# Kernel optimization log

Hardware: AMD Instinct MI355X
Metric: run time of the kernel (lower is better)

The kernel has to match this reference:

```python
import jax, jax.numpy as jnp
import numpy as np

NUM_EMBED = 1024
NUM_HEADS = 16
NUM_LAYER = 8
BLOCK_SIZE = 1024
VOCAB = 32000
B, T = 4, 1024
HEAD_SIZE = NUM_EMBED // NUM_HEADS


def _ln(x, g, b, eps=1e-5):
    mu = jnp.mean(x, axis=-1, keepdims=True)
    var = jnp.var(x, axis=-1, keepdims=True)
    return (x - mu) * jax.lax.rsqrt(var + eps) * g + b


def setup_inputs() -> dict:
    key = jax.random.key(0)
    ks = jax.random.split(key, 16)
    C, L, V = NUM_EMBED, NUM_LAYER, VOCAB
    std = 0.02
    n = lambda k, shp: jax.random.normal(k, shp, jnp.float32) * std
    return {
        "x": jax.random.randint(ks[0], (B, T), 0, V),
        "tok_emb": n(ks[1], (V, C)),
        "pos_emb": n(ks[2], (BLOCK_SIZE, C)),
        "Wq": n(ks[3], (L, C, C)),
        "Wk": n(ks[4], (L, C, C)),
        "Wv": n(ks[5], (L, C, C)),
        "Wproj": n(ks[6], (L, C, C)),
        "bproj": jnp.zeros((L, C), jnp.float32),
        "ln1_g": jnp.ones((L, C), jnp.float32),
        "ln1_b": jnp.zeros((L, C), jnp.float32),
        "ln2_g": jnp.ones((L, C), jnp.float32),
        "ln2_b": jnp.zeros((L, C), jnp.float32),
        "W1": n(ks[7], (L, C, 4 * C)),
        "b1": jnp.zeros((L, 4 * C), jnp.float32),
        "W2": n(ks[8], (L, 4 * C, C)),
        "b2": jnp.zeros((L, C), jnp.float32),
        "lnf_g": jnp.ones((C,), jnp.float32),
        "lnf_b": jnp.zeros((C,), jnp.float32),
        "Whead": n(ks[9], (C, V)),
    }


def _forward(x, tok_emb, pos_emb, Wq, Wk, Wv, Wproj, bproj,
             ln1_g, ln1_b, ln2_g, ln2_b, W1, b1, W2, b2,
             lnf_g, lnf_b, Whead):
    Bc, Tc = x.shape
    H, hs = NUM_HEADS, HEAD_SIZE
    h = tok_emb[x] + pos_emb[:Tc]  # [B,T,C]
    causal = jnp.tril(jnp.ones((Tc, Tc), bool))
    neg_inf = jnp.finfo(h.dtype).min
    for l in range(NUM_LAYER):
        xn = _ln(h, ln1_g[l], ln1_b[l])
        q = (xn @ Wq[l]).reshape(Bc, Tc, H, hs)
        k = (xn @ Wk[l]).reshape(Bc, Tc, H, hs)
        v = (xn @ Wv[l]).reshape(Bc, Tc, H, hs)
        att = jnp.einsum('bqhd,bkhd->bhqk', q, k) * (hs ** -0.5)
        att = jnp.where(causal, att, neg_inf)
        att = jax.nn.softmax(att, axis=-1)  # dropout p=0 in eval
        o = jnp.einsum('bhqk,bkhd->bqhd', att, v).reshape(Bc, Tc, H * hs)
        h = h + o @ Wproj[l] + bproj[l]
        xn = _ln(h, ln2_g[l], ln2_b[l])
        h = h + jax.nn.relu(xn @ W1[l] + b1[l]) @ W2[l] + b2[l]
    h = _ln(h, lnf_g, lnf_b)
    return h @ Whead  # logits [B,T,V]


def reference(x, tok_emb, pos_emb, Wq, Wk, Wv, Wproj, bproj,
              ln1_g, ln1_b, ln2_g, ln2_b, W1, b1, W2, b2,
              lnf_g, lnf_b, Whead):
    return _forward(x, tok_emb, pos_emb, Wq, Wk, Wv, Wproj, bproj,
                    ln1_g, ln1_b, ln2_g, ln2_b, W1, b1, W2, b2,
                    lnf_g, lnf_b, Whead)
```

## Files before the change

kernel.cpp:

```cpp
#include <hip/hip_runtime.h>
#include <stdint.h>
#include <stddef.h>

#define C_DIM 1024
#define T_DIM 1024
#define B_DIM 4
#define L_DIM 8
#define V_DIM 32000
#define HS 64
#define NHEAD 16
#define NROWS (B_DIM * T_DIM)
#define LDQ   3072

typedef __bf16 bf16_t;
typedef __attribute__((ext_vector_type(8))) __bf16 bf16x8;
typedef __attribute__((ext_vector_type(4))) __bf16 bf16x4;
typedef __attribute__((ext_vector_type(4))) float f32x4;
typedef unsigned int u32;
typedef unsigned short u16;

static __device__ __forceinline__ f32x4 mfma16(bf16x8 a, bf16x8 b, f32x4 c) {
    return __builtin_amdgcn_mfma_f32_16x16x32_bf16(a, b, c, 0, 0, 0);
}

static __device__ __forceinline__ void gl_lds16(const bf16_t* g, bf16_t* l) {
    __builtin_amdgcn_global_load_lds(
        (const __attribute__((address_space(1))) u32*)(const void*)g,
        (__attribute__((address_space(3))) u32*)(void*)l, 16, 0, 0);
}

__global__ __launch_bounds__(256) void embed_kernel(
    const int* __restrict__ x, const float* __restrict__ tok,
    const float* __restrict__ pos, float* __restrict__ h) {
    int idx = blockIdx.x * 256 + threadIdx.x;
    int row = idx >> 8;
    int c4  = (idx & 255) * 4;
    int t   = row & (T_DIM - 1);
    int tk  = x[row];
    float4 a = *(const float4*)(tok + (size_t)tk * C_DIM + c4);
    float4 p = *(const float4*)(pos + (size_t)t * C_DIM + c4);
    float4 r;
    r.x = a.x + p.x; r.y = a.y + p.y; r.z = a.z + p.z; r.w = a.w + p.w;
    *(float4*)(h + (size_t)row * C_DIM + c4) = r;
}

static __device__ __forceinline__ void wtr_tile(
    const float* __restrict__ in, bf16_t* __restrict__ out,
    int K, int N, int n0, int k0, int tid) {
    __shared__ float t[64][65];
    int tx = tid & 63, tw = tid >> 6;
#pragma unroll 4
    for (int i = 0; i < 16; ++i) {
        int k = tw * 16 + i;
        t[k][tx] = in[(size_t)(k0 + k) * N + n0 + tx];
    }
    __syncthreads();
#pragma unroll 4
    for (int i = 0; i < 16; ++i) {
        int n = tw * 16 + i;
        out[(size_t)(n0 + n) * K + k0 + tx] = (bf16_t)t[tx][n];
    }
}

__global__ __launch_bounds__(256) void wtr_kernel(
    const float* __restrict__ in, bf16_t* __restrict__ out, int K, int N) {
    wtr_tile(in, out, K, N, blockIdx.x * 64, blockIdx.y * 64, threadIdx.x);
}

__global__ __launch_bounds__(256) void wtr_layer_kernel(
    const float* __restrict__ Wq, const float* __restrict__ Wk,
    const float* __restrict__ Wv, const float* __restrict__ Wp,
    const float* __restrict__ W1, const float* __restrict__ W2,
    bf16_t* __restrict__ qkvT, bf16_t* __restrict__ projT,
    bf16_t* __restrict__ w1T, bf16_t* __restrict__ w2T) {
    int b = blockIdx.x;
    const float* in; bf16_t* out; int K, N, tn, tk;
    if (b < 1024) {
        int which = b >> 8, t = b & 255;
        in  = which == 0 ? Wq : which == 1 ? Wk : which == 2 ? Wv : Wp;
        out = which < 3 ? qkvT + (size_t)which * C_DIM * C_DIM : projT;
        K = C_DIM; N = C_DIM; tn = t & 15; tk = t >> 4;
    } else if (b < 2048) {
        int t = b - 1024; in = W1; out = w1T;
        K = C_DIM; N = 4 * C_DIM; tn = t & 63; tk = t >> 6;
    } else {
        int t = b - 2048; in = W2; out = w2T;
        K = 4 * C_DIM; N = C_DIM; tn = t & 15; tk = t >> 4;
    }
    wtr_tile(in, out, K, N, tn * 64, tk * 64, threadIdx.x);
}

__global__ __launch_bounds__(256) void ln_kernel(
    const float* __restrict__ x, const float* __restrict__ gam,
    const float* __restrict__ bet, bf16_t* __restrict__ out) {
    int wave = threadIdx.x >> 6, lane = threadIdx.x & 63;
    int row  = blockIdx.x * 4 + wave;
    const float* xr = x + (size_t)row * C_DIM;
    float4 v[4];
    float s = 0.f, sq = 0.f;
#pragma unroll
    for (int i = 0; i < 4; ++i) {
        v[i] = *(const float4*)(xr + i * 256 + lane * 4);
        s  += v[i].x + v[i].y + v[i].z + v[i].w;
        sq += v[i].x * v[i].x + v[i].y * v[i].y + v[i].z * v[i].z + v[i].w * v[i].w;
    }
#pragma unroll
    for (int m = 1; m < 64; m <<= 1) {
        s  += __shfl_xor(s, m);
        sq += __shfl_xor(sq, m);
    }
    float mu  = s * (1.f / 1024.f);
    float var = sq * (1.f / 1024.f) - mu * mu;
    float rs  = rsqrtf(var + 1e-5f);
    bf16_t* orow = out + (size_t)row * C_DIM;
#pragma unroll
    for (int i = 0; i < 4; ++i) {
        int c = i * 256 + lane * 4;
        float4 g4 = *(const float4*)(gam + c);
        float4 b4 = *(const float4*)(bet + c);
        bf16x4 o;
        o[0] = (bf16_t)((v[i].x - mu) * rs * g4.x + b4.x);
        o[1] = (bf16_t)((v[i].y - mu) * rs * g4.y + b4.y);
        o[2] = (bf16_t)((v[i].z - mu) * rs * g4.z + b4.z);
        o[3] = (bf16_t)((v[i].w - mu) * rs * g4.w + b4.w);
        *(bf16x4*)(orow + c) = o;
    }
}

template <int MODE>
__global__ __launch_bounds__(256) void gemm_kernel(
    const bf16_t* __restrict__ A, const bf16_t* __restrict__ Bt,
    const float* __restrict__ bias, void* __restrict__ Cout,
    int M, int N, int K) {
    __shared__ bf16_t Asm[2][128 * 32];
    __shared__ bf16_t Bsm[2][128 * 32];

    const int tid  = threadIdx.x;
    const int nwg  = gridDim.x;
    int bid = blockIdx.x;
    if ((nwg & 7) == 0) {
        int cpx = nwg >> 3;
        bid = (bid & 7) * cpx + (bid >> 3);
    }
    const int MT = M >> 7;
    const int mt = bid % MT, nt = bid / MT;
    const int mbase = mt << 7, nbase = nt << 7;
    const int wave = tid >> 6, lane = tid & 63;
    const int lr = lane & 15, lg = lane >> 4;
    const int wm = wave >> 1, wn = wave & 1;
    const int NK = K >> 5;

    const int srow = lane >> 2;
    const int ssw  = (((lane & 3) ^ ((lane >> 3) & 3)) << 3);
    const bf16_t* aRow = A  + (size_t)(mbase + wave * 32 + srow) * K + ssw;
    const bf16_t* bRow = Bt + (size_t)(nbase + wave * 32 + srow) * K + ssw;
    const int ldsW = wave * 1024;

#define STAGE(buf, kt)                                                        \
    do {                                                                      \
        const bf16_t* ag = aRow + (size_t)(kt) * 32;                          \
        const bf16_t* bg = bRow + (size_t)(kt) * 32;                          \
        gl_lds16(ag,            &Asm[buf][ldsW]);                             \
        gl_lds16(ag + 16 * K,   &Asm[buf][ldsW + 512]);                       \
        gl_lds16(bg,            &Bsm[buf][ldsW]);                             \
        gl_lds16(bg + 16 * K,   &Bsm[buf][ldsW + 512]);                       \
    } while (0)

    STAGE(0, 0);
    __syncthreads();

    f32x4 acc[4][4] = {};
    const int rsw = ((lg ^ ((lr >> 1) & 3)) << 3);
    int buf = 0;
    for (int kt = 0; kt < NK; ++kt) {
        if (kt + 1 < NK) STAGE(buf ^ 1, kt + 1);
        bf16x8 af[4], bfr[4];
#pragma unroll
        for (int i = 0; i < 4; ++i)
            af[i] = *(const bf16x8*)&Asm[buf][(wm * 64 + i * 16 + lr) * 32 + rsw];
#pragma unroll
        for (int j = 0; j < 4; ++j)
            bfr[j] = *(const bf16x8*)&Bsm[buf][(wn * 64 + j * 16 + lr) * 32 + rsw];
#pragma unroll
        for (int i = 0; i < 4; ++i)
#pragma unroll
            for (int j = 0; j < 4; ++j)
                acc[i][j] = mfma16(af[i], bfr[j], acc[i][j]);
        __syncthreads();
        buf ^= 1;
    }
#undef STAGE

    float bj[4];
#pragma unroll
    for (int j = 0; j < 4; ++j)
        bj[j] = bias ? bias[nbase + wn * 64 + j * 16 + lr] : 0.0f;
#pragma unroll
    for (int i = 0; i < 4; ++i) {
#pragma unroll
        for (int j = 0; j < 4; ++j) {
            int col = nbase + wn * 64 + j * 16 + lr;
#pragma unroll
            for (int e = 0; e < 4; ++e) {
                int row = mbase + wm * 64 + i * 16 + lg * 4 + e;
                float val = acc[i][j][e] + bj[j];
                size_t off = (size_t)row * N + col;
                if (MODE == 0) {
                    ((bf16_t*)Cout)[off] = (bf16_t)val;
                } else if (MODE == 1) {
                    ((bf16_t*)Cout)[off] = (bf16_t)fmaxf(val, 0.0f);
                } else if (MODE == 2) {
                    ((float*)Cout)[off] += val;
                } else {
                    __builtin_nontemporal_store(val, &((float*)Cout)[off]);
                }
            }
        }
    }
}

__global__ __launch_bounds__(256) void attn_kernel(
    const bf16_t* __restrict__ Qb, const bf16_t* __restrict__ Kb,
    const bf16_t* __restrict__ Vb, bf16_t* __restrict__ Ob) {
    __shared__ bf16_t Ksm[2][64][72];
    __shared__ bf16_t Vsm[2][64][72];
    __shared__ bf16_t Psm[4][32][72];

    const int tid  = threadIdx.x;
    const int bid  = blockIdx.x;
    const int qt   = 7 - (bid >> 6);
    const int bh   = bid & 63;
    const int hh   = bh & 15;
    const int bb   = bh >> 4;
    const int wave = tid >> 6, lane = tid & 63;
    const int lr = lane & 15, lg = lane >> 4;
    const int qbase = qt * 128 + wave * 32;
    const size_t basei = ((size_t)bb * T_DIM) * LDQ + hh * HS;
    const size_t baseo = ((size_t)bb * T_DIM) * C_DIM + hh * HS;

    bf16x8 qf[2][2];
#pragma unroll
    for (int rb = 0; rb < 2; ++rb) {
        const bf16_t* qrow = Qb + basei + (size_t)(qbase + rb * 16 + lr) * LDQ;
        qf[rb][0] = *(const bf16x8*)(qrow + lg * 8);
        qf[rb][1] = *(const bf16x8*)(qrow + 32 + lg * 8);
    }

    f32x4 o[2][4] = {};
    float m_run[2][4], psum[2][4];
#pragma unroll
    for (int rb = 0; rb < 2; ++rb)
#pragma unroll
        for (int e = 0; e < 4; ++e) { m_run[rb][e] = -1e30f; psum[rb][e] = 0.f; }

    const int krow = tid >> 2, kc = (tid & 3) * 8;
    const bf16_t* kgp = Kb + basei + (size_t)krow * LDQ + kc;
    const int vds = (tid & 7) * 8, vkg = (tid >> 3) * 2;
    const bf16_t* vgp0 = Vb + basei + (size_t)vkg * LDQ + vds;
    const bf16_t* vgp1 = vgp0 + LDQ;

    const int nkt = 2 * qt + 2;

    uint4 k0r, k1r, v0r, v1r;
    k0r = *(const uint4*)(kgp);
    k1r = *(const uint4*)(kgp + 32);
    v0r = *(const uint4*)(vgp0);
    v1r = *(const uint4*)(vgp1);
    *(uint4*)&Ksm[0][krow][kc]      = k0r;
    *(uint4*)&Ksm[0][krow][kc + 32] = k1r;
    {
        const u16* e0 = (const u16*)&v0r;
        const u16* e1 = (const u16*)&v1r;
#pragma unroll
        for (int j = 0; j < 8; ++j)
            *(u32*)&Vsm[0][vds + j][vkg] = (u32)e0[j] | ((u32)e1[j] << 16);
    }
    __syncthreads();

    const float SCL = 0.18033688011112042f;
    for (int kt = 0; kt < nkt; ++kt) {
        const int c = kt & 1;
        if (kt + 1 < nkt) {
            const size_t go = (size_t)(kt + 1) * 64 * LDQ;
            k0r = *(const uint4*)(kgp + go);
            k1r = *(const uint4*)(kgp + go + 32);
            v0r = *(const uint4*)(vgp0 + go);
            v1r = *(const uint4*)(vgp1 + go);
        }

        f32x4 s[2][4];
        __builtin_amdgcn_s_setprio(1);
#pragma unroll
        for (int kk = 0; kk < 4; ++kk) {
            bf16x8 kf0 = *(const bf16x8*)&Ksm[c][kk * 16 + lr][lg * 8];
            bf16x8 kf1 = *(const bf16x8*)&Ksm[c][kk * 16 + lr][32 + lg * 8];
#pragma unroll
            for (int rb = 0; rb < 2; ++rb) {
                f32x4 z = {};
                z = mfma16(qf[rb][0], kf0, z);
                z = mfma16(qf[rb][1], kf1, z);
                s[rb][kk] = z;
            }
        }
        __builtin_amdgcn_s_setprio(0);
        if (kt * 64 + 63 > qbase) {
#pragma unroll
            for (int rb = 0; rb < 2; ++rb)
#pragma unroll
                for (int kk = 0; kk < 4; ++kk)
#pragma unroll
                    for (int e = 0; e < 4; ++e) {
                        int key = kt * 64 + kk * 16 + lr;
                        int qi  = qbase + rb * 16 + lg * 4 + e;
                        float v = s[rb][kk][e] * SCL;
                        s[rb][kk][e] = (key <= qi) ? v : -1e30f;
                    }
        } else {
#pragma unroll
            for (int rb = 0; rb < 2; ++rb)
#pragma unroll
                for (int kk = 0; kk < 4; ++kk)
#pragma unroll
                    for (int e = 0; e < 4; ++e)
                        s[rb][kk][e] *= SCL;
        }

#pragma unroll
        for (int rb = 0; rb < 2; ++rb) {
#pragma unroll
            for (int e = 0; e < 4; ++e) {
                float v = fmaxf(fmaxf(s[rb][0][e], s[rb][1][e]),
                                fmaxf(s[rb][2][e], s[rb][3][e]));
                v = fmaxf(v, __shfl_xor(v, 1));
                v = fmaxf(v, __shfl_xor(v, 2));
                v = fmaxf(v, __shfl_xor(v, 4));
                v = fmaxf(v, __shfl_xor(v, 8));
                float mo = m_run[rb][e];
                if (v > mo + 8.f) {
                    float alpha = exp2f(mo - v);
                    m_run[rb][e] = v;
                    psum[rb][e] *= alpha;
#pragma unroll
                    for (int db = 0; db < 4; ++db)
                        o[rb][db][e] *= alpha;
                }
                float mn = m_run[rb][e];
                float p0 = exp2f(s[rb][0][e] - mn);
                float p1 = exp2f(s[rb][1][e] - mn);
                float p2 = exp2f(s[rb][2][e] - mn);
                float p3 = exp2f(s[rb][3][e] - mn);
                int qrow = rb * 16 + lg * 4 + e;
                Psm[wave][qrow][lr]      = (bf16_t)p0;
                Psm[wave][qrow][16 + lr] = (bf16_t)p1;
                Psm[wave][qrow][32 + lr] = (bf16_t)p2;
                Psm[wave][qrow][48 + lr] = (bf16_t)p3;
                psum[rb][e] += (p0 + p1) + (p2 + p3);
            }
        }

        asm volatile("s_waitcnt lgkmcnt(0)" ::: "memory");
        bf16x8 pf[2][2];
#pragma unroll
        for (int rb = 0; rb < 2; ++rb)
#pragma unroll
            for (int h2 = 0; h2 < 2; ++h2)
                pf[rb][h2] = *(const bf16x8*)&Psm[wave][rb * 16 + lr][h2 * 32 + lg * 8];
        __builtin_amdgcn_s_setprio(1);
#pragma unroll
        for (int h2 = 0; h2 < 2; ++h2)
#pragma unroll
            for (int db = 0; db < 4; ++db) {
                bf16x8 vf = *(const bf16x8*)&Vsm[c][db * 16 + lr][h2 * 32 + lg * 8];
#pragma unroll
                for (int rb = 0; rb < 2; ++rb)
                    o[rb][db] = mfma16(pf[rb][h2], vf, o[rb][db]);
            }
        __builtin_amdgcn_s_setprio(0);

        if (kt + 1 < nkt) {
            const int w = c ^ 1;
            *(uint4*)&Ksm[w][krow][kc]      = k0r;
            *(uint4*)&Ksm[w][krow][kc + 32] = k1r;
            const u16* e0 = (const u16*)&v0r;
            const u16* e1 = (const u16*)&v1r;
#pragma unroll
            for (int j = 0; j < 8; ++j)
                *(u32*)&Vsm[w][vds + j][vkg] = (u32)e0[j] | ((u32)e1[j] << 16);
        }
        __syncthreads();
    }

#pragma unroll
    for (int rb = 0; rb < 2; ++rb)
#pragma unroll
        for (int e = 0; e < 4; ++e) {
            float l = psum[rb][e];
            l += __shfl_xor(l, 1);
            l += __shfl_xor(l, 2);
            l += __shfl_xor(l, 4);
            l += __shfl_xor(l, 8);
            float inv = 1.0f / l;
            bf16_t* orow = Ob + baseo + (size_t)(qbase + rb * 16 + lg * 4 + e) * C_DIM;
#pragma unroll
            for (int db = 0; db < 4; ++db)
                orow[db * 16 + lr] = (bf16_t)(o[rb][db][e] * inv);
        }
}

extern "C" void kernel_launch(void* const* d_in, const int* in_sizes, int n_in,
                              void* d_out, int out_size, void* d_ws, size_t ws_size,
                              hipStream_t stream) {
    const int*   x      = (const int*)d_in[0];
    const float* tok    = (const float*)d_in[1];
    const float* pos    = (const float*)d_in[2];
    const float* Wq     = (const float*)d_in[3];
    const float* Wk     = (const float*)d_in[4];
    const float* Wv     = (const float*)d_in[5];
    const float* Wproj  = (const float*)d_in[6];
    const float* bproj  = (const float*)d_in[7];
    const float* ln1_g  = (const float*)d_in[8];
    const float* ln1_b  = (const float*)d_in[9];
    const float* ln2_g  = (const float*)d_in[10];
    const float* ln2_b  = (const float*)d_in[11];
    const float* W1     = (const float*)d_in[12];
    const float* b1     = (const float*)d_in[13];
    const float* W2     = (const float*)d_in[14];
    const float* b2     = (const float*)d_in[15];
    const float* lnf_g  = (const float*)d_in[16];
    const float* lnf_b  = (const float*)d_in[17];
    const float* Whead  = (const float*)d_in[18];
    float* out = (float*)d_out;

    char* ws = (char*)d_ws;
    float*  h    = (float*)ws;   ws += (size_t)NROWS * C_DIM * 4;
    bf16_t* xn   = (bf16_t*)ws;  ws += (size_t)NROWS * C_DIM * 2;
    bf16_t* qkvb = (bf16_t*)ws;  ws += (size_t)NROWS * LDQ * 2;
    bf16_t* ob   = (bf16_t*)ws;  ws += (size_t)NROWS * C_DIM * 2;
    bf16_t* mid  = (bf16_t*)ws;  ws += (size_t)NROWS * 4 * C_DIM * 2;
    bf16_t* wT   = (bf16_t*)ws;  ws += (size_t)V_DIM * C_DIM * 2;

    const size_t M1 = (size_t)C_DIM * C_DIM;
    bf16_t* qkvT  = wT;
    bf16_t* projT = wT + 3 * M1;
    bf16_t* w1T   = wT + 4 * M1;
    bf16_t* w2T   = wT + 8 * M1;

    dim3 blk(256);

    embed_kernel<<<dim3(NROWS * C_DIM / 1024), blk, 0, stream>>>(x, tok, pos, h);

    for (int l = 0; l < L_DIM; ++l) {
        const size_t wo  = (size_t)l * M1;
        const size_t wo1 = (size_t)l * 4 * M1;

        wtr_layer_kernel<<<dim3(3072), blk, 0, stream>>>(
            Wq + wo, Wk + wo, Wv + wo, Wproj + wo, W1 + wo1, W2 + wo1,
            qkvT, projT, w1T, w2T);

        ln_kernel<<<dim3(NROWS / 4), blk, 0, stream>>>(h, ln1_g + l * C_DIM, ln1_b + l * C_DIM, xn);

        gemm_kernel<0><<<dim3(32 * 24), blk, 0, stream>>>(xn, qkvT, nullptr, qkvb, NROWS, LDQ, C_DIM);

        attn_kernel<<<dim3(B_DIM * NHEAD * (T_DIM / 128)), blk, 0, stream>>>(
            qkvb, qkvb + C_DIM, qkvb + 2 * C_DIM, ob);

        gemm_kernel<2><<<dim3(32 * 8), blk, 0, stream>>>(ob, projT, bproj + l * C_DIM, h, NROWS, C_DIM, C_DIM);

        ln_kernel<<<dim3(NROWS / 4), blk, 0, stream>>>(h, ln2_g + l * C_DIM, ln2_b + l * C_DIM, xn);

        gemm_kernel<1><<<dim3(32 * 32), blk, 0, stream>>>(xn, w1T, b1 + (size_t)l * 4 * C_DIM, mid, NROWS, 4 * C_DIM, C_DIM);
        gemm_kernel<2><<<dim3(32 * 8), blk, 0, stream>>>(mid, w2T, b2 + l * C_DIM, h, NROWS, C_DIM, 4 * C_DIM);
    }

    ln_kernel<<<dim3(NROWS / 4), blk, 0, stream>>>(h, lnf_g, lnf_b, xn);
    wtr_kernel<<<dim3(500, 16), blk, 0, stream>>>(Whead, wT, C_DIM, V_DIM);
    gemm_kernel<3><<<dim3(32 * 250), blk, 0, stream>>>(xn, wT, nullptr, out, NROWS, V_DIM, C_DIM);
}
```

Baseline: 2.760 ms.

## Add 256x256-tile GEMM kernel for FFN-up and LM-head projections

Introduces a 512-thread GEMM with 256x256 output tiles, double-buffered LDS loaded by direct global-to-LDS copies, an XOR-swizzled LDS layout, prefetch interleaved with MFMA sub-steps, and an XCD-aware block remap. It is used for the W1 (ReLU) GEMM and the vocabulary head GEMM in place of the smaller-tile kernel. Larger tiles raise arithmetic intensity and cut global traffic per FLOP. In exchange, each block uses 64KB of LDS, the grid for W1 shrinks to 256 blocks, and the extra barriers per K-step could limit overlap.

After: 2.677 ms. 3.0% less time.

```diff
diff --git a/kernel.cpp b/kernel.cpp
--- a/kernel.cpp
+++ b/kernel.cpp
@@ -211,6 +211,121 @@
                     ((bf16_t*)Cout)[off] = (bf16_t)fmaxf(val, 0.0f);
                 } else if (MODE == 2) {
                     ((float*)Cout)[off] += val;
+                } else {
+                    __builtin_nontemporal_store(val, &((float*)Cout)[off]);
+                }
+            }
+        }
+    }
+}
+
+template <int MODE>
+__global__ __launch_bounds__(512, 2) void gemm256_kernel(
+    const bf16_t* __restrict__ A, const bf16_t* __restrict__ Bt,
+    const float* __restrict__ bias, void* __restrict__ Cout,
+    int M, int N, int K) {
+    __shared__ bf16_t As[2][256 * 64];
+    __shared__ bf16_t Bs[2][256 * 64];
+
+    const int tid  = threadIdx.x;
+    const int nwg  = gridDim.x;
+    int bid = blockIdx.x;
+    if ((nwg & 7) == 0) {
+        int cpx = nwg >> 3;
+        bid = (bid & 7) * cpx + (bid >> 3);
+    }
+    const int MT = M >> 8;
+    const int mt = bid % MT, nt = bid / MT;
+    const int mbase = mt << 8, nbase = nt << 8;
+    const int wave = tid >> 6, lane = tid & 63;
+    const int lr = lane & 15, lg = lane >> 4;
+    const int wm128 = (wave >> 2) * 128;
+    const int wn64  = (wave & 3) * 64;
+    const int NT = K >> 6;
+
+    const int ssw = (((tid & 7) ^ ((tid >> 3) & 7)) << 3);
+    const bf16_t* aRow = A  + (size_t)(mbase + (tid >> 3)) * K + ssw;
+    const bf16_t* bRow = Bt + (size_t)(nbase + (tid >> 3)) * K + ssw;
+    const int ldsW = wave * 8 * 64;
+
+#pragma unroll
+    for (int i = 0; i < 4; ++i) {
+        gl_lds16(aRow + (size_t)i * 64 * K, &As[0][i * 64 * 64 + ldsW]);
+        gl_lds16(bRow + (size_t)i * 64 * K, &Bs[0][i * 64 * 64 + ldsW]);
+    }
+    asm volatile("s_waitcnt vmcnt(0)" ::: "memory");
+    __builtin_amdgcn_s_barrier();
+    asm volatile("" ::: "memory");
+
+    f32x4 acc[8][4] = {};
+
+    for (int t = 0; t < NT; ++t) {
+        const int cur = t & 1, nxt = cur ^ 1;
+        const bool pf = (t + 1 < NT);
+#pragma unroll
+        for (int q = 0; q < 4; ++q) {
+            bf16x8 af[2][2], bfr[2][4];
+#pragma unroll
+            for (int h = 0; h < 2; ++h) {
+                const int c = h * 4 + lg;
+#pragma unroll
+                for (int dm = 0; dm < 2; ++dm) {
+                    int row = wm128 + (2 * q + dm) * 16 + lr;
+                    af[h][dm] = *(const bf16x8*)
+                        &As[cur][row * 64 + ((c ^ (row & 7)) << 3)];
+                }
+#pragma unroll
+                for (int nf = 0; nf < 4; ++nf) {
+                    int row = wn64 + nf * 16 + lr;
+                    bfr[h][nf] = *(const bf16x8*)
+                        &Bs[cur][row * 64 + ((c ^ (row & 7)) << 3)];
+                }
+            }
+            if (q < 2 && pf) {
+#pragma unroll
+                for (int i = 2 * q; i < 2 * q + 2; ++i) {
+                    gl_lds16(aRow + (size_t)(t + 1) * 64 + (size_t)i * 64 * K,
+                             &As[nxt][i * 64 * 64 + ldsW]);
+                    gl_lds16(bRow + (size_t)(t + 1) * 64 + (size_t)i * 64 * K,
+                             &Bs[nxt][i * 64 * 64 + ldsW]);
+                }
+            }
+            __builtin_amdgcn_s_barrier();
+            asm volatile("" ::: "memory");
+            __builtin_amdgcn_s_setprio(1);
+#pragma unroll
+            for (int h = 0; h < 2; ++h)
+#pragma unroll
+                for (int dm = 0; dm < 2; ++dm)
+#pragma unroll
+                    for (int nf = 0; nf < 4; ++nf)
+                        acc[2 * q + dm][nf] =
+                            mfma16(af[h][dm], bfr[h][nf], acc[2 * q + dm][nf]);
+            __builtin_amdgcn_s_setprio(0);
+            __builtin_amdgcn_s_barrier();
+            asm volatile("" ::: "memory");
+        }
+        if (pf) asm volatile("s_waitcnt vmcnt(0)" ::: "memory");
+        __builtin_amdgcn_s_barrier();
+        asm volatile("" ::: "memory");
+    }
+
+    float bj[4];
+#pragma unroll
+    for (int nf = 0; nf < 4; ++nf)
+        bj[nf] = bias ? bias[nbase + wn64 + nf * 16 + lr] : 0.0f;
+#pragma unroll
+    for (int mf = 0; mf < 8; ++mf) {
+#pragma unroll
+        for (int nf = 0; nf < 4; ++nf) {
+            int col = nbase + wn64 + nf * 16 + lr;
+#pragma unroll
+            for (int e = 0; e < 4; ++e) {
+                int row = mbase + wm128 + mf * 16 + lg * 4 + e;
+                float val = acc[mf][nf][e] + bj[nf];
+                size_t off = (size_t)row * N + col;
+                if (MODE == 1) {
+                    ((bf16_t*)Cout)[off] = (bf16_t)fmaxf(val, 0.0f);
                 } else {
                     __builtin_nontemporal_store(val, &((float*)Cout)[off]);
                 }
@@ -446,6 +561,7 @@
     bf16_t* w2T   = wT + 8 * M1;
 
     dim3 blk(256);
+    dim3 blk512(512);
 
     embed_kernel<<<dim3(NROWS * C_DIM / 1024), blk, 0, stream>>>(x, tok, pos, h);
 
@@ -468,11 +584,13 @@
 
         ln_kernel<<<dim3(NROWS / 4), blk, 0, stream>>>(h, ln2_g + l * C_DIM, ln2_b + l * C_DIM, xn);
 
-        gemm_kernel<1><<<dim3(32 * 32), blk, 0, stream>>>(xn, w1T, b1 + (size_t)l * 4 * C_DIM, mid, NROWS, 4 * C_DIM, C_DIM);
+        gemm256_kernel<1><<<dim3(16 * 16), blk512, 0, stream>>>(
+            xn, w1T, b1 + (size_t)l * 4 * C_DIM, mid, NROWS, 4 * C_DIM, C_DIM);
         gemm_kernel<2><<<dim3(32 * 8), blk, 0, stream>>>(mid, w2T, b2 + l * C_DIM, h, NROWS, C_DIM, 4 * C_DIM);
     }
 
     ln_kernel<<<dim3(NROWS / 4), blk, 0, stream>>>(h, lnf_g, lnf_b, xn);
     wtr_kernel<<<dim3(500, 16), blk, 0, stream>>>(Whead, wT, C_DIM, V_DIM);
-    gemm_kernel<3><<<dim3(32 * 250), blk, 0, stream>>>(xn, wT, nullptr, out, NROWS, V_DIM, C_DIM);
-}
+    gemm256_kernel<3><<<dim3(16 * 125), blk512, 0, stream>>>(
+        xn, wT, nullptr, out, NROWS, V_DIM, C_DIM);
+}
```

## Add 128x256-tile 512-thread GEMM for FFN-up and LM-head projections

Applied to the files above, without the earlier changes.

Adds a wider GEMM kernel with 8 waves per block and a 128x256 output tile, staged through double-buffered swizzled LDS with direct global-to-LDS loads. It replaces the 256-thread GEMM for the W1 (ReLU) projection and the vocabulary head, halving the block count. The aim is more reuse of each A tile across a wider N tile, cutting global and LDS traffic per MFMA. The larger shared-memory footprint and register use may lower occupancy, and the head GEMM's N of 32000 must divide evenly by 256, which it does (125 tiles).

Result: faster. 2.645 ms (-4.2%).

```diff
diff --git a/kernel.cpp b/kernel.cpp
--- a/kernel.cpp
+++ b/kernel.cpp
@@ -211,6 +211,94 @@
                     ((bf16_t*)Cout)[off] = (bf16_t)fmaxf(val, 0.0f);
                 } else if (MODE == 2) {
                     ((float*)Cout)[off] += val;
+                } else {
+                    __builtin_nontemporal_store(val, &((float*)Cout)[off]);
+                }
+            }
+        }
+    }
+}
+
+template <int MODE>
+__global__ __launch_bounds__(512, 4) void gemmW_kernel(
+    const bf16_t* __restrict__ A, const bf16_t* __restrict__ Bt,
+    const float* __restrict__ bias, void* __restrict__ Cout,
+    int M, int N, int K) {
+    __shared__ bf16_t As[2][128 * 32];
+    __shared__ bf16_t Bs[2][256 * 32];
+
+    const int tid  = threadIdx.x;
+    const int nwg  = gridDim.x;
+    int bid = blockIdx.x;
+    if ((nwg & 7) == 0) {
+        int cpx = nwg >> 3;
+        bid = (bid & 7) * cpx + (bid >> 3);
+    }
+    const int MT = M >> 7;
+    const int mt = bid % MT, nt = bid / MT;
+    const int mbase = mt << 7, nbase = nt << 8;
+    const int wave = tid >> 6, lane = tid & 63;
+    const int lr = lane & 15, lg = lane >> 4;
+    const int wm64 = (wave >> 2) * 64;
+    const int wn64 = (wave & 3) * 64;
+    const int NK = K >> 5;
+
+    const int srow = tid >> 2;
+    const int csrc = (((tid & 3) ^ ((srow & 3) ^ ((srow >> 2) & 3))) << 3);
+    const bf16_t* aPtr = A  + (size_t)(mbase + srow) * K + csrc;
+    const bf16_t* b0   = Bt + (size_t)(nbase + srow) * K + csrc;
+    const bf16_t* b1   = b0 + (size_t)128 * K;
+    const int ldsW = wave * 512;
+
+#define STAGEW(buf, kt)                                                       \
+    do {                                                                      \
+        gl_lds16(aPtr + (size_t)(kt) * 32, &As[buf][ldsW]);                   \
+        gl_lds16(b0   + (size_t)(kt) * 32, &Bs[buf][ldsW]);                   \
+        gl_lds16(b1   + (size_t)(kt) * 32, &Bs[buf][4096 + ldsW]);            \
+    } while (0)
+
+    STAGEW(0, 0);
+    __syncthreads();
+
+    f32x4 acc[4][4] = {};
+    const int rsw = (lr & 3) ^ ((lr >> 2) & 3);
+    const int rofs = ((lg ^ rsw) << 3);
+    int buf = 0;
+    for (int kt = 0; kt < NK; ++kt) {
+        if (kt + 1 < NK) STAGEW(buf ^ 1, kt + 1);
+        bf16x8 af[4], bfr[4];
+#pragma unroll
+        for (int i = 0; i < 4; ++i)
+            af[i] = *(const bf16x8*)&As[buf][(wm64 + i * 16 + lr) * 32 + rofs];
+#pragma unroll
+        for (int j = 0; j < 4; ++j)
+            bfr[j] = *(const bf16x8*)&Bs[buf][(wn64 + j * 16 + lr) * 32 + rofs];
+#pragma unroll
+        for (int i = 0; i < 4; ++i)
+#pragma unroll
+            for (int j = 0; j < 4; ++j)
+                acc[i][j] = mfma16(af[i], bfr[j], acc[i][j]);
+        __syncthreads();
+        buf ^= 1;
+    }
+#undef STAGEW
+
+    float bj[4];
+#pragma unroll
+    for (int j = 0; j < 4; ++j)
+        bj[j] = bias ? bias[nbase + wn64 + j * 16 + lr] : 0.0f;
+#pragma unroll
+    for (int i = 0; i < 4; ++i) {
+#pragma unroll
+        for (int j = 0; j < 4; ++j) {
+            int col = nbase + wn64 + j * 16 + lr;
+#pragma unroll
+            for (int e = 0; e < 4; ++e) {
+                int row = mbase + wm64 + i * 16 + lg * 4 + e;
+                float val = acc[i][j][e] + bj[j];
+                size_t off = (size_t)row * N + col;
+                if (MODE == 1) {
+                    ((bf16_t*)Cout)[off] = (bf16_t)fmaxf(val, 0.0f);
                 } else {
                     __builtin_nontemporal_store(val, &((float*)Cout)[off]);
                 }
@@ -446,6 +534,7 @@
     bf16_t* w2T   = wT + 8 * M1;
 
     dim3 blk(256);
+    dim3 blk512(512);
 
     embed_kernel<<<dim3(NROWS * C_DIM / 1024), blk, 0, stream>>>(x, tok, pos, h);
 
@@ -468,11 +557,13 @@
 
         ln_kernel<<<dim3(NROWS / 4), blk, 0, stream>>>(h, ln2_g + l * C_DIM, ln2_b + l * C_DIM, xn);
 
-        gemm_kernel<1><<<dim3(32 * 32), blk, 0, stream>>>(xn, w1T, b1 + (size_t)l * 4 * C_DIM, mid, NROWS, 4 * C_DIM, C_DIM);
+        gemmW_kernel<1><<<dim3(32 * 16), blk512, 0, stream>>>(
+            xn, w1T, b1 + (size_t)l * 4 * C_DIM, mid, NROWS, 4 * C_DIM, C_DIM);
         gemm_kernel<2><<<dim3(32 * 8), blk, 0, stream>>>(mid, w2T, b2 + l * C_DIM, h, NROWS, C_DIM, 4 * C_DIM);
     }
 
     ln_kernel<<<dim3(NROWS / 4), blk, 0, stream>>>(h, lnf_g, lnf_b, xn);
     wtr_kernel<<<dim3(500, 16), blk, 0, stream>>>(Whead, wT, C_DIM, V_DIM);
-    gemm_kernel<3><<<dim3(32 * 250), blk, 0, stream>>>(xn, wT, nullptr, out, NROWS, V_DIM, C_DIM);
-}
+    gemmW_kernel<3><<<dim3(32 * 125), blk512, 0, stream>>>(
+        xn, wT, nullptr, out, NROWS, V_DIM, C_DIM);
+}
```
